# Performance work log

Hardware: AMD Instinct MI355X
Metric: run time of the kernel (lower is better)

Reference implementation:

```python
import jax, jax.numpy as jnp
import numpy as np

B, S, H = 8, 8192, 1024
CAPACITY_FACTOR = 0.5


def setup_inputs() -> dict:
    key = jax.random.key(0)
    ks = jax.random.split(key, 5)
    sc = lambda fan: np.float32(1.0 / np.sqrt(fan))
    return {
        "x": jax.random.normal(ks[0], (B, S, H), dtype=jnp.float32),
        # router: Linear(H, H//4) -> ReLU -> Linear(H//4, 1)
        "W1": jax.random.normal(ks[1], (H, H // 4), dtype=jnp.float32) * sc(H),
        "b1": jnp.zeros((H // 4,), dtype=jnp.float32),
        "W2": jax.random.normal(ks[2], (H // 4, 1), dtype=jnp.float32) * sc(H // 4),
        "b2": jnp.zeros((1,), dtype=jnp.float32),
        # external layer_fn realized as a dense layer: gelu(x @ Wl)
        "Wl": jax.random.normal(ks[3], (H, H), dtype=jnp.float32) * sc(H),
    }


def reference(x, W1, b1, W2, b2, Wl):
    # router scores [B, S, 1]
    scores = jax.nn.relu(jnp.einsum("bsh,hd->bsd", x, W1) + b1)
    scores = jnp.einsum("bsd,do->bso", scores, W2) + b2
    routing_weights = jax.nn.sigmoid(scores)  # [B, S, 1]

    # eval path: process only top-capacity tokens per batch row
    capacity = int(S * CAPACITY_FACTOR)
    _, top_idx = jax.lax.top_k(scores[..., 0], capacity)  # [B, C]

    selected = jnp.take_along_axis(x, top_idx[..., None], axis=1)  # [B, C, H]
    processed = jax.nn.gelu(jnp.einsum("bch,hd->bcd", selected, Wl))  # layer_fn

    batch_idx = jnp.arange(x.shape[0])[:, None]  # [B, 1]
    output = x.at[batch_idx, top_idx].set(processed)  # scatter back into clone of x
    return output, routing_weights
```

## Files before the change

### kernel.cpp

```cpp
#include <hip/hip_runtime.h>
#include <stdint.h>

#define B_   8
#define S_   8192
#define H_   1024
#define HQ_  256
#define CAP_ 4096
#define UCAP_ (S_-CAP_)
#define M_   (B_*CAP_)
#define EPSB 2e-3f
#define LCAP 8192

using f32x4 = __attribute__((ext_vector_type(4))) float;
using s16x8 = __attribute__((ext_vector_type(8))) short;

__device__ __forceinline__ unsigned short f2bf(float f) {
  unsigned u = __float_as_uint(f);
  u += 0x7FFF + ((u >> 16) & 1);
  return (unsigned short)(u >> 16);
}
__device__ __forceinline__ float bf2f(unsigned short h) {
  return __uint_as_float(((unsigned)h) << 16);
}

__device__ __forceinline__ float gelu_f(float v) {
  float s = v + 0.044715f * v * v * v;
  float e = __expf(-1.5957691216057308f * s);
  return v * __builtin_amdgcn_rcpf(1.0f + e);
}

__device__ __forceinline__ unsigned mono(float f) {
  unsigned u = __float_as_uint(f);
  return (u & 0x80000000u) ? ~u : (u | 0x80000000u);
}
__device__ __forceinline__ float unmono(unsigned k) {
  unsigned u = (k & 0x80000000u) ? (k & 0x7fffffffu) : ~k;
  return __uint_as_float(u);
}

__device__ __forceinline__ void gload_lds16(const void* g, void* l) {
  __builtin_amdgcn_global_load_lds(
      (const __attribute__((address_space(1))) void*)(uintptr_t)g,
      (__attribute__((address_space(3))) void*)(uintptr_t)l,
      16, 0, 0);
}

__global__ __launch_bounds__(256) void prep_w1_kernel(
    const float* __restrict__ W1, unsigned short* __restrict__ w1t_hi,
    unsigned short* __restrict__ w1t_lo) {
  __shared__ float tile[32][33];
  const int n0 = blockIdx.x * 32, k0 = blockIdx.y * 32;
  const int tx = threadIdx.x, ty = threadIdx.y;
  for (int i = ty; i < 32; i += 8) tile[i][tx] = W1[(size_t)(k0 + i) * HQ_ + n0 + tx];
  __syncthreads();
  for (int i = ty; i < 32; i += 8) {
    float v = tile[tx][i];
    unsigned short h = f2bf(v);
    w1t_hi[(size_t)(n0 + i) * H_ + k0 + tx] = h;
    w1t_lo[(size_t)(n0 + i) * H_ + k0 + tx] = f2bf(v - bf2f(h));
  }
}

__global__ __launch_bounds__(512) void router_mfma_kernel(
    const float* __restrict__ x, const unsigned short* __restrict__ w1t_hi,
    const unsigned short* __restrict__ w1t_lo, const float* __restrict__ b1,
    const float* __restrict__ W2, const float* __restrict__ b2,
    float* __restrict__ scores) {
  __shared__ __align__(16) unsigned short AsH[128 * 32];
  __shared__ __align__(16) unsigned short AsL[128 * 32];
  __shared__ __align__(16) unsigned short BsH[256 * 32];
  __shared__ __align__(16) unsigned short BsL[256 * 32];
  __shared__ float part[128][4];
  const int t = threadIdx.x;
  const int lane = t & 63, w = t >> 6;
  const int m0 = blockIdx.x * 128;
  const int wr = w >> 2, wc = w & 3;
  const int r16 = lane & 15, ks = lane >> 4;

  f32x4 acc[4][4];
  #pragma unroll
  for (int i = 0; i < 4; ++i)
    #pragma unroll
    for (int j = 0; j < 4; ++j) acc[i][j] = (f32x4){0.f, 0.f, 0.f, 0.f};

  for (int k0 = 0; k0 < H_; k0 += 32) {
    #pragma unroll
    for (int u = 0; u < 2; ++u) {
      int idx = t + u * 512;
      int row = idx >> 3, q = idx & 7;
      float4 v = *(const float4*)&x[(size_t)(m0 + row) * H_ + k0 + q * 4];
      ushort4 hh, ll;
      hh.x = f2bf(v.x); ll.x = f2bf(v.x - bf2f(hh.x));
      hh.y = f2bf(v.y); ll.y = f2bf(v.y - bf2f(hh.y));
      hh.z = f2bf(v.z); ll.z = f2bf(v.z - bf2f(hh.z));
      hh.w = f2bf(v.w); ll.w = f2bf(v.w - bf2f(hh.w));
      int so = row * 32 + (((q >> 1) ^ (row & 3)) << 3) + (q & 1) * 4;
      *(ushort4*)&AsH[so] = hh;
      *(ushort4*)&AsL[so] = ll;
    }
    #pragma unroll
    for (int q = 0; q < 2; ++q) {
      int c0 = (q * 8 + w) * 64;
      int g = c0 + lane;
      int row = g >> 2, sl = g & 3;
      int slz = sl ^ (row & 3);
      gload_lds16(&w1t_hi[(size_t)row * H_ + k0 + slz * 8], &BsH[c0 * 8]);
      gload_lds16(&w1t_lo[(size_t)row * H_ + k0 + slz * 8], &BsL[c0 * 8]);
    }
    __syncthreads();
    s16x8 ah[4], al[4], bh[4], bl[4];
    #pragma unroll
    for (int i = 0; i < 4; ++i) {
      int r = wr * 64 + i * 16 + r16;
      int co = (ks ^ (r & 3)) * 8;
      ah[i] = *(const s16x8*)&AsH[r * 32 + co];
      al[i] = *(const s16x8*)&AsL[r * 32 + co];
    }
    #pragma unroll
    for (int j = 0; j < 4; ++j) {
      int r = wc * 64 + j * 16 + r16;
      int co = (ks ^ (r & 3)) * 8;
      bh[j] = *(const s16x8*)&BsH[r * 32 + co];
      bl[j] = *(const s16x8*)&BsL[r * 32 + co];
    }
    #pragma unroll
    for (int i = 0; i < 4; ++i)
      #pragma unroll
      for (int j = 0; j < 4; ++j) {
        acc[i][j] = __builtin_amdgcn_mfma_f32_16x16x32_bf16(ah[i], bh[j], acc[i][j], 0, 0, 0);
        acc[i][j] = __builtin_amdgcn_mfma_f32_16x16x32_bf16(ah[i], bl[j], acc[i][j], 0, 0, 0);
        acc[i][j] = __builtin_amdgcn_mfma_f32_16x16x32_bf16(al[i], bh[j], acc[i][j], 0, 0, 0);
      }
    __syncthreads();
  }

  float b1v[4], w2v[4];
  #pragma unroll
  for (int j = 0; j < 4; ++j) {
    int n = wc * 64 + j * 16 + r16;
    b1v[j] = b1[n]; w2v[j] = W2[n];
  }
  const int g4 = lane >> 4;
  #pragma unroll
  for (int i = 0; i < 4; ++i) {
    #pragma unroll
    for (int r = 0; r < 4; ++r) {
      float p = 0.f;
      #pragma unroll
      for (int j = 0; j < 4; ++j) {
        float h = acc[i][j][r] + b1v[j];
        h = fmaxf(h, 0.f);
        p = fmaf(h, w2v[j], p);
      }
      p += __shfl_xor(p, 1);
      p += __shfl_xor(p, 2);
      p += __shfl_xor(p, 4);
      p += __shfl_xor(p, 8);
      if (r16 == 0) part[wr * 64 + i * 16 + g4 * 4 + r][wc] = p;
    }
  }
  __syncthreads();
  if (t < 128)
    scores[m0 + t] = part[t][0] + part[t][1] + part[t][2] + part[t][3] + b2[0];
}

__global__ __launch_bounds__(1024) void select_kernel(
    const float* __restrict__ scores, float* __restrict__ thr) {
  __shared__ unsigned hist[2048];
  __shared__ unsigned sh_b, sh_gt;
  const int b = blockIdx.x;
  const int tid = threadIdx.x;
  const float* srow = scores + (size_t)b * S_;
  unsigned prefix = 0; int plen = 0; unsigned rank = CAP_;
  #pragma unroll
  for (int round = 0; round < 3; ++round) {
    const int nb = (round < 2) ? 11 : 10;
    hist[tid] = 0; hist[tid + 1024] = 0;
    __syncthreads();
    for (int i = tid; i < S_; i += 1024) {
      unsigned k = mono(srow[i]);
      if (plen == 0 || (k >> (32 - plen)) == prefix) {
        unsigned bucket = (k << plen) >> (32 - nb);
        atomicAdd(&hist[bucket], 1u);
      }
    }
    __syncthreads();
    for (int s = 1; s < 2048; s <<= 1) {
      unsigned t0 = (tid + s < 2048) ? hist[tid + s] : 0;
      unsigned t1 = (tid + 1024 + s < 2048) ? hist[tid + 1024 + s] : 0;
      __syncthreads();
      hist[tid] += t0; hist[tid + 1024] += t1;
      __syncthreads();
    }
    #pragma unroll
    for (int h = 0; h < 2; ++h) {
      int i = tid + h * 1024;
      unsigned ge = hist[i];
      unsigned gt = (i < 2047) ? hist[i + 1] : 0;
      if (gt < rank && rank <= ge) { sh_b = (unsigned)i; sh_gt = gt; }
    }
    __syncthreads();
    prefix = (prefix << nb) | sh_b;
    plen += nb;
    rank -= sh_gt;
    __syncthreads();
  }
  if (tid == 0) thr[b] = unmono(prefix);
}

__global__ __launch_bounds__(256) void band_kernel(
    const float* __restrict__ scores, const float* __restrict__ thr,
    int* __restrict__ list, int* __restrict__ count) {
  int i = blockIdx.x * 256 + threadIdx.x;
  float s = scores[i];
  int b = i >> 13;
  if (fabsf(s - thr[b]) <= EPSB) {
    int p = atomicAdd(count, 1);
    if (p < LCAP) list[p] = i;
  }
}

__global__ __launch_bounds__(256) void recompute_kernel(
    const float* __restrict__ x, const float* __restrict__ W1,
    const float* __restrict__ b1, const float* __restrict__ W2,
    const float* __restrict__ b2, const int* __restrict__ list,
    const int* __restrict__ count, float* __restrict__ scores) {
  __shared__ float xr[H_];
  __shared__ float red[4];
  int n = *count; if (n > LCAP) n = LCAP;
  const int j = threadIdx.x;
  for (int li = blockIdx.x; li < n; li += gridDim.x) {
    int tok = list[li];
    const float* xrow = x + (size_t)tok * H_;
    for (int k = j; k < H_; k += 256) xr[k] = xrow[k];
    __syncthreads();
    float a = 0.f;
    for (int k = 0; k < H_; ++k) a = fmaf(xr[k], W1[(size_t)k * HQ_ + j], a);
    float h = fmaxf(a + b1[j], 0.f);
    float v = h * W2[j];
    v += __shfl_xor(v, 1);  v += __shfl_xor(v, 2);  v += __shfl_xor(v, 4);
    v += __shfl_xor(v, 8);  v += __shfl_xor(v, 16); v += __shfl_xor(v, 32);
    if ((j & 63) == 0) red[j >> 6] = v;
    __syncthreads();
    if (j == 0) scores[tok] = red[0] + red[1] + red[2] + red[3] + b2[0];
    __syncthreads();
  }
}

__global__ __launch_bounds__(1024) void compact_kernel(
    const float* __restrict__ scores, const float* __restrict__ thr,
    int* __restrict__ comp, int* __restrict__ ucomp) {
  __shared__ int wc_eq[16], wc_sel[16], red[16];
  const int b = blockIdx.x;
  const float T = thr[b];
  const float* srow = scores + (size_t)b * S_;
  const int tid = threadIdx.x, lane = tid & 63, wid = tid >> 6;

  int cgt = 0;
  #pragma unroll
  for (int c = 0; c < 8; ++c) cgt += (srow[c * 1024 + tid] > T) ? 1 : 0;
  cgt += __shfl_xor(cgt, 1);  cgt += __shfl_xor(cgt, 2);  cgt += __shfl_xor(cgt, 4);
  cgt += __shfl_xor(cgt, 8);  cgt += __shfl_xor(cgt, 16); cgt += __shfl_xor(cgt, 32);
  if (lane == 0) red[wid] = cgt;
  __syncthreads();
  int cnt_gt = 0;
  #pragma unroll
  for (int i = 0; i < 16; ++i) cnt_gt += red[i];
  const int need = CAP_ - cnt_gt;

  int* crow = comp + b * CAP_;
  int* urow = ucomp + b * UCAP_;
  int sel_base = 0, unsel_base = 0, eq_base = 0;
  __syncthreads();
  for (int c = 0; c < 8; ++c) {
    int idx = c * 1024 + tid;
    float s = srow[idx];
    bool gt = s > T, eq = (s == T);
    unsigned long long meq = __ballot(eq);
    if (lane == 0) wc_eq[wid] = __popcll(meq);
    __syncthreads();
    int eq_off = eq_base, eq_tot = 0;
    #pragma unroll
    for (int w2 = 0; w2 < 16; ++w2) { if (w2 < wid) eq_off += wc_eq[w2]; eq_tot += wc_eq[w2]; }
    int eqpos = eq_off + __popcll(meq & ((1ull << lane) - 1));
    bool take = gt || (eq && eqpos < need);
    unsigned long long mt = __ballot(take);
    if (lane == 0) wc_sel[wid] = __popcll(mt);
    __syncthreads();
    int sel_off = sel_base, sel_tot = 0;
    #pragma unroll
    for (int w2 = 0; w2 < 16; ++w2) { if (w2 < wid) sel_off += wc_sel[w2]; sel_tot += wc_sel[w2]; }
    if (take) {
      crow[sel_off + __popcll(mt & ((1ull << lane) - 1))] = idx;
    } else {
      int un_off = unsel_base + wid * 64 - (sel_off - sel_base);
      urow[un_off + __popcll(~mt & ((1ull << lane) - 1))] = idx;
    }
    sel_base += sel_tot; unsel_base += 1024 - sel_tot; eq_base += eq_tot;
    __syncthreads();
  }
}

__global__ __launch_bounds__(256) void rw_kernel(
    const float* __restrict__ scores, float* __restrict__ rw) {
  int i = blockIdx.x * 256 + threadIdx.x;
  rw[i] = 1.f / (1.f + expf(-scores[i]));
}

__global__ __launch_bounds__(256) void copy_unsel_kernel(
    const float* __restrict__ x, const int* __restrict__ ucomp,
    float* __restrict__ out) {
  int i = blockIdx.x;
  int b = i >> 12, r = i & (UCAP_ - 1);
  int token = ucomp[b * UCAP_ + r];
  size_t row = (size_t)b * S_ + token;
  const float4* src = (const float4*)(x + row * H_);
  float4* dst = (float4*)(out + row * H_);
  dst[threadIdx.x] = src[threadIdx.x];
}

__global__ __launch_bounds__(256) void wlt_kernel(
    const float* __restrict__ wl, unsigned short* __restrict__ wlt) {
  __shared__ float tile[32][33];
  const int x0 = blockIdx.x * 32, y0 = blockIdx.y * 32;
  const int tx = threadIdx.x, ty = threadIdx.y;
  for (int i = ty; i < 32; i += 8) tile[i][tx] = wl[(size_t)(y0 + i) * H_ + x0 + tx];
  __syncthreads();
  for (int i = ty; i < 32; i += 8)
    wlt[(size_t)(x0 + i) * H_ + y0 + tx] = f2bf(tile[tx][i]);
}

__global__ __launch_bounds__(256) void gather_cast_kernel(
    const float* __restrict__ x, const int* __restrict__ comp,
    unsigned short* __restrict__ xg) {
  int tid = blockIdx.x * 256 + threadIdx.x;
  int rowc = tid >> 8;
  int c4 = tid & 255;
  int b = rowc >> 12, cc = rowc & (CAP_ - 1);
  int token = comp[b * CAP_ + cc];
  float4 v = *(const float4*)&x[((size_t)(b * S_ + token)) * H_ + c4 * 4];
  ushort4 o;
  o.x = f2bf(v.x); o.y = f2bf(v.y); o.z = f2bf(v.z); o.w = f2bf(v.w);
  *(ushort4*)&xg[(size_t)rowc * H_ + c4 * 4] = o;
}

__global__ __launch_bounds__(256) void moe_gemm_kernel(
    const unsigned short* __restrict__ xg, const unsigned short* __restrict__ wlt,
    const int* __restrict__ comp, float* __restrict__ out) {
  __shared__ __align__(16) unsigned short As[128 * 64];
  __shared__ __align__(16) unsigned short Bs[128 * 64];
  __shared__ int toks[128];
  const int t = threadIdx.x;
  const int lane = t & 63, w = t >> 6;
  const int n0 = blockIdx.x * 128, m0 = blockIdx.y * 128;
  const int bb = m0 >> 12;
  if (t < 128) toks[t] = comp[bb * CAP_ + (m0 & (CAP_ - 1)) + t];
  const int wr = w >> 1, wc = w & 1;
  const int r16 = lane & 15, ks = lane >> 4;

  const unsigned short* aS[4];
  const unsigned short* bS[4];
  #pragma unroll
  for (int u = 0; u < 4; ++u) {
    int c = u * 256 + t;
    int row = c >> 3, sl = c & 7;
    int slz = sl ^ (row & 7);
    aS[u] = xg + (size_t)(m0 + row) * H_ + slz * 8;
    bS[u] = wlt + (size_t)(n0 + row) * H_ + slz * 8;
  }

  f32x4 acc[4][4];
  #pragma unroll
  for (int i = 0; i < 4; ++i)
    #pragma unroll
    for (int j = 0; j < 4; ++j) acc[i][j] = (f32x4){0.f, 0.f, 0.f, 0.f};

  for (int k0 = 0; k0 < H_; k0 += 64) {
    #pragma unroll
    for (int u = 0; u < 4; ++u) {
      gload_lds16(aS[u] + k0, &As[(u * 256 + w * 64) * 8]);
      gload_lds16(bS[u] + k0, &Bs[(u * 256 + w * 64) * 8]);
    }
    __syncthreads();
    #pragma unroll
    for (int kk = 0; kk < 2; ++kk) {
      s16x8 af[4], bfr[4];
      const int g = kk * 4 + ks;
      #pragma unroll
      for (int i = 0; i < 4; ++i) {
        int r = wr * 64 + i * 16 + r16;
        af[i] = *(const s16x8*)&As[r * 64 + (g ^ (r & 7)) * 8];
      }
      #pragma unroll
      for (int j = 0; j < 4; ++j) {
        int r = wc * 64 + j * 16 + r16;
        bfr[j] = *(const s16x8*)&Bs[r * 64 + (g ^ (r & 7)) * 8];
      }
      #pragma unroll
      for (int i = 0; i < 4; ++i)
        #pragma unroll
        for (int j = 0; j < 4; ++j)
          acc[i][j] = __builtin_amdgcn_mfma_f32_16x16x32_bf16(af[i], bfr[j], acc[i][j], 0, 0, 0);
    }
    __syncthreads();
  }

  #pragma unroll
  for (int i = 0; i < 4; ++i) {
    #pragma unroll
    for (int r = 0; r < 4; ++r) {
      int rl = wr * 64 + i * 16 + (lane >> 4) * 4 + r;
      int token = toks[rl];
      float* orow = out + ((size_t)(bb * S_ + token)) * H_ + n0 + wc * 64;
      #pragma unroll
      for (int j = 0; j < 4; ++j)
        orow[j * 16 + r16] = gelu_f(acc[i][j][r]);
    }
  }
}

extern "C" void kernel_launch(void* const* d_in, const int* in_sizes, int n_in,
                              void* d_out, int out_size, void* d_ws, size_t ws_size,
                              hipStream_t stream) {
  const float* x  = (const float*)d_in[0];
  const float* W1 = (const float*)d_in[1];
  const float* b1 = (const float*)d_in[2];
  const float* W2 = (const float*)d_in[3];
  const float* b2 = (const float*)d_in[4];
  const float* Wl = (const float*)d_in[5];
  float* out = (float*)d_out;
  float* rw  = out + (size_t)B_ * S_ * H_;

  char* ws = (char*)d_ws;
  float* scores        = (float*)ws;
  int*   comp          = (int*)(ws + (256 << 10));
  float* thr           = (float*)(ws + (384 << 10));
  int*   count         = (int*)(ws + (384 << 10) + 256);
  int*   list          = (int*)(ws + (384 << 10) + 512);
  int*   ucomp         = (int*)(ws + (448 << 10));
  unsigned short* wlt  = (unsigned short*)(ws + (1 << 20));
  unsigned short* xg   = (unsigned short*)(ws + (3 << 20));
  unsigned short* w1t_hi = xg;
  unsigned short* w1t_lo = xg + 262144;

  hipMemsetAsync(count, 0, sizeof(int), stream);
  hipLaunchKernelGGL(prep_w1_kernel, dim3(HQ_/32, H_/32), dim3(32, 8), 0, stream,
                     W1, w1t_hi, w1t_lo);
  hipLaunchKernelGGL(router_mfma_kernel, dim3((B_*S_)/128), dim3(512), 0, stream,
                     x, w1t_hi, w1t_lo, b1, W2, b2, scores);
  hipLaunchKernelGGL(select_kernel, dim3(B_), dim3(1024), 0, stream, scores, thr);
  hipLaunchKernelGGL(band_kernel, dim3((B_*S_)/256), dim3(256), 0, stream,
                     scores, thr, list, count);
  hipLaunchKernelGGL(recompute_kernel, dim3(256), dim3(256), 0, stream,
                     x, W1, b1, W2, b2, list, count, scores);
  hipLaunchKernelGGL(select_kernel, dim3(B_), dim3(1024), 0, stream, scores, thr);
  hipLaunchKernelGGL(compact_kernel, dim3(B_), dim3(1024), 0, stream,
                     scores, thr, comp, ucomp);
  hipLaunchKernelGGL(rw_kernel, dim3((B_*S_)/256), dim3(256), 0, stream,
                     scores, rw);
  hipLaunchKernelGGL(copy_unsel_kernel, dim3(B_*UCAP_), dim3(256), 0, stream,
                     x, ucomp, out);
  hipLaunchKernelGGL(wlt_kernel, dim3(H_/32, H_/32), dim3(32, 8), 0, stream, Wl, wlt);
  hipLaunchKernelGGL(gather_cast_kernel, dim3(M_*H_/4/256), dim3(256), 0, stream,
                     x, comp, xg);
  hipLaunchKernelGGL(moe_gemm_kernel, dim3(H_/128, M_/128), dim3(256), 0, stream,
                     xg, wlt, comp, out);
}
```

Measured before the change: 425.8 us.

## Drop x low-part MFMA in router, batch recompute tokens, XCD-aware GEMM block mapping

The router GEMM no longer splits x into bf16 hi/lo parts. It runs two MFMAs per tile instead of three, which removes one LDS buffer and its conversion work. To compensate for the lower score precision, the near-threshold band is widened, so more tokens are sent to the exact fp32 recompute. The recompute kernel now handles four tokens per block so each W1 load is shared across them. The MoE GEMM launch is flattened into one dimension and remapped so that each XCD works on contiguous M rows, which should improve L2 locality. The risk is that the wider band and larger recompute list may not absorb every ordering error from the cheaper router.

Result: faster. 417.2 us (-2.0%).

```diff
diff --git a/kernel.cpp b/kernel.cpp
--- a/kernel.cpp
+++ b/kernel.cpp
@@ -8,7 +8,7 @@
 #define CAP_ 4096
 #define UCAP_ (S_-CAP_)
 #define M_   (B_*CAP_)
-#define EPSB 2e-3f
+#define EPSB 5e-3f
 #define LCAP 8192
 
 using f32x4 = __attribute__((ext_vector_type(4))) float;
@@ -67,7 +67,6 @@
     const float* __restrict__ W2, const float* __restrict__ b2,
     float* __restrict__ scores) {
   __shared__ __align__(16) unsigned short AsH[128 * 32];
-  __shared__ __align__(16) unsigned short AsL[128 * 32];
   __shared__ __align__(16) unsigned short BsH[256 * 32];
   __shared__ __align__(16) unsigned short BsL[256 * 32];
   __shared__ float part[128][4];
@@ -89,14 +88,10 @@
       int idx = t + u * 512;
       int row = idx >> 3, q = idx & 7;
       float4 v = *(const float4*)&x[(size_t)(m0 + row) * H_ + k0 + q * 4];
-      ushort4 hh, ll;
-      hh.x = f2bf(v.x); ll.x = f2bf(v.x - bf2f(hh.x));
-      hh.y = f2bf(v.y); ll.y = f2bf(v.y - bf2f(hh.y));
-      hh.z = f2bf(v.z); ll.z = f2bf(v.z - bf2f(hh.z));
-      hh.w = f2bf(v.w); ll.w = f2bf(v.w - bf2f(hh.w));
+      ushort4 hh;
+      hh.x = f2bf(v.x); hh.y = f2bf(v.y); hh.z = f2bf(v.z); hh.w = f2bf(v.w);
       int so = row * 32 + (((q >> 1) ^ (row & 3)) << 3) + (q & 1) * 4;
       *(ushort4*)&AsH[so] = hh;
-      *(ushort4*)&AsL[so] = ll;
     }
     #pragma unroll
     for (int q = 0; q < 2; ++q) {
@@ -108,13 +103,12 @@
       gload_lds16(&w1t_lo[(size_t)row * H_ + k0 + slz * 8], &BsL[c0 * 8]);
     }
     __syncthreads();
-    s16x8 ah[4], al[4], bh[4], bl[4];
+    s16x8 ah[4], bh[4], bl[4];
     #pragma unroll
     for (int i = 0; i < 4; ++i) {
       int r = wr * 64 + i * 16 + r16;
       int co = (ks ^ (r & 3)) * 8;
       ah[i] = *(const s16x8*)&AsH[r * 32 + co];
-      al[i] = *(const s16x8*)&AsL[r * 32 + co];
     }
     #pragma unroll
     for (int j = 0; j < 4; ++j) {
@@ -129,7 +123,6 @@
       for (int j = 0; j < 4; ++j) {
         acc[i][j] = __builtin_amdgcn_mfma_f32_16x16x32_bf16(ah[i], bh[j], acc[i][j], 0, 0, 0);
         acc[i][j] = __builtin_amdgcn_mfma_f32_16x16x32_bf16(ah[i], bl[j], acc[i][j], 0, 0, 0);
-        acc[i][j] = __builtin_amdgcn_mfma_f32_16x16x32_bf16(al[i], bh[j], acc[i][j], 0, 0, 0);
       }
     __syncthreads();
   }
@@ -225,24 +218,38 @@
     const float* __restrict__ b1, const float* __restrict__ W2,
     const float* __restrict__ b2, const int* __restrict__ list,
     const int* __restrict__ count, float* __restrict__ scores) {
-  __shared__ float xr[H_];
-  __shared__ float red[4];
+  __shared__ float xr[4][H_];
+  __shared__ float red[4][4];
   int n = *count; if (n > LCAP) n = LCAP;
   const int j = threadIdx.x;
-  for (int li = blockIdx.x; li < n; li += gridDim.x) {
-    int tok = list[li];
-    const float* xrow = x + (size_t)tok * H_;
-    for (int k = j; k < H_; k += 256) xr[k] = xrow[k];
-    __syncthreads();
-    float a = 0.f;
-    for (int k = 0; k < H_; ++k) a = fmaf(xr[k], W1[(size_t)k * HQ_ + j], a);
-    float h = fmaxf(a + b1[j], 0.f);
-    float v = h * W2[j];
-    v += __shfl_xor(v, 1);  v += __shfl_xor(v, 2);  v += __shfl_xor(v, 4);
-    v += __shfl_xor(v, 8);  v += __shfl_xor(v, 16); v += __shfl_xor(v, 32);
-    if ((j & 63) == 0) red[j >> 6] = v;
-    __syncthreads();
-    if (j == 0) scores[tok] = red[0] + red[1] + red[2] + red[3] + b2[0];
+  for (int base = blockIdx.x * 4; base < n; base += gridDim.x * 4) {
+    int nt = n - base; if (nt > 4) nt = 4;
+    for (int tt = 0; tt < 4; ++tt) {
+      int tok = list[base + ((tt < nt) ? tt : 0)];
+      const float* xrow = x + (size_t)tok * H_;
+      for (int k = j; k < H_; k += 256) xr[tt][k] = xrow[k];
+    }
+    __syncthreads();
+    float a0 = 0.f, a1 = 0.f, a2 = 0.f, a3 = 0.f;
+    for (int k = 0; k < H_; ++k) {
+      float wv = W1[(size_t)k * HQ_ + j];
+      a0 = fmaf(xr[0][k], wv, a0);
+      a1 = fmaf(xr[1][k], wv, a1);
+      a2 = fmaf(xr[2][k], wv, a2);
+      a3 = fmaf(xr[3][k], wv, a3);
+    }
+    float aa[4] = {a0, a1, a2, a3};
+    #pragma unroll
+    for (int tt = 0; tt < 4; ++tt) {
+      float h = fmaxf(aa[tt] + b1[j], 0.f);
+      float v = h * W2[j];
+      v += __shfl_xor(v, 1);  v += __shfl_xor(v, 2);  v += __shfl_xor(v, 4);
+      v += __shfl_xor(v, 8);  v += __shfl_xor(v, 16); v += __shfl_xor(v, 32);
+      if ((j & 63) == 0) red[tt][j >> 6] = v;
+    }
+    __syncthreads();
+    if (j < nt)
+      scores[list[base + j]] = red[j][0] + red[j][1] + red[j][2] + red[j][3] + b2[0];
     __syncthreads();
   }
 }
@@ -352,7 +359,10 @@
   __shared__ int toks[128];
   const int t = threadIdx.x;
   const int lane = t & 63, w = t >> 6;
-  const int n0 = blockIdx.x * 128, m0 = blockIdx.y * 128;
+  const int bid = blockIdx.x;
+  const int xcd = bid & 7, wl_ = bid >> 3;
+  const int m0 = (xcd * 32 + (wl_ >> 3)) * 128;
+  const int n0 = (wl_ & 7) * 128;
   const int bb = m0 >> 12;
   if (t < 128) toks[t] = comp[bb * CAP_ + (m0 & (CAP_ - 1)) + t];
   const int wr = w >> 1, wc = w & 1;
@@ -451,7 +461,7 @@
   hipLaunchKernelGGL(select_kernel, dim3(B_), dim3(1024), 0, stream, scores, thr);
   hipLaunchKernelGGL(band_kernel, dim3((B_*S_)/256), dim3(256), 0, stream,
                      scores, thr, list, count);
-  hipLaunchKernelGGL(recompute_kernel, dim3(256), dim3(256), 0, stream,
+  hipLaunchKernelGGL(recompute_kernel, dim3(128), dim3(256), 0, stream,
                      x, W1, b1, W2, b2, list, count, scores);
   hipLaunchKernelGGL(select_kernel, dim3(B_), dim3(1024), 0, stream, scores, thr);
   hipLaunchKernelGGL(compact_kernel, dim3(B_), dim3(1024), 0, stream,
@@ -463,6 +473,6 @@
   hipLaunchKernelGGL(wlt_kernel, dim3(H_/32, H_/32), dim3(32, 8), 0, stream, Wl, wlt);
   hipLaunchKernelGGL(gather_cast_kernel, dim3(M_*H_/4/256), dim3(256), 0, stream,
                      x, comp, xg);
-  hipLaunchKernelGGL(moe_gemm_kernel, dim3(H_/128, M_/128), dim3(256), 0, stream,
+  hipLaunchKernelGGL(moe_gemm_kernel, dim3((M_/128)*(H_/128)), dim3(256), 0, stream,
                      xg, wlt, comp, out);
 }
```
